# Performance work log

Hardware: AMD Instinct MI355X
Metric: run time of the kernel (lower is better)

## Reference

```python
import jax, jax.numpy as jnp
import numpy as np

H = 1024        # hidden_size
I = 512         # moe_intermediate_size
E = 16          # n_routed_experts
K = 2           # num_experts_per_tok
N_SHARED = 2    # n_shared_experts
IS = I * N_SHARED  # shared expert intermediate
B, S = 2, 2048


def setup_inputs() -> dict:
    key = jax.random.key(0)
    ks = jax.random.split(key, 9)
    sc = 0.02
    return {
        "hidden_states": jax.random.normal(ks[0], (B, S, H), jnp.float32),
        "router_w":     jax.random.normal(ks[1], (E, H), jnp.float32) * sc,
        "expert_gate":  jax.random.normal(ks[2], (E, H, I), jnp.float32) * sc,
        "expert_up":    jax.random.normal(ks[3], (E, H, I), jnp.float32) * sc,
        "expert_down":  jax.random.normal(ks[4], (E, I, H), jnp.float32) * sc,
        "shared_gate":  jax.random.normal(ks[5], (H, IS), jnp.float32) * sc,
        "shared_up":    jax.random.normal(ks[6], (H, IS), jnp.float32) * sc,
        "shared_down":  jax.random.normal(ks[7], (IS, H), jnp.float32) * sc,
    }


def reference(hidden_states, router_w, expert_gate, expert_up, expert_down,
              shared_gate, shared_up, shared_down):
    orig_shape = hidden_states.shape
    x = hidden_states.reshape(-1, H)            # [T, H]
    T = x.shape[0]

    # --- MoEGate: softmax router scores, top-k, normalized weights ---
    scores = jax.nn.softmax(x @ router_w.T, axis=-1)        # [T, E]
    topk_w, topk_idx = jax.lax.top_k(scores, K)             # [T, K]
    topk_w = topk_w / jnp.sum(topk_w, axis=-1, keepdims=True)  # norm_topk_prob

    # Sparse combine weights as dense [T, E] gate matrix (scatter of top-k).
    gates = jnp.zeros((T, E), x.dtype).at[jnp.arange(T)[:, None], topk_idx].add(topk_w)

    # --- Routed experts: gated SiLU MLP per expert, weighted combine ---
    g = jnp.einsum('th,ehi->tei', x, expert_gate)           # [T, E, I]
    u = jnp.einsum('th,ehi->tei', x, expert_up)             # [T, E, I]
    a = jax.nn.silu(g) * u                                  # [T, E, I]
    y = jnp.einsum('tei,eih,te->th', a, expert_down, gates) # [T, H]

    # --- Shared experts ---
    s = (jax.nn.silu(x @ shared_gate) * (x @ shared_up)) @ shared_down  # [T, H]

    return (y + s).reshape(orig_shape)
```

## Files before the change

kernel.cpp:

```cpp
#include <hip/hip_runtime.h>
#include <math.h>

#define H_DIM 1024
#define I_DIM 512
#define E_NUM 16
#define T_TOK 4096
#define IS_DIM 1024
#define CSTR 32

#define P_RT   1024
#define P_WU   (P_RT + 2048)
#define P_SG   (P_WU + 2048)
#define P_SU   (P_SG + 256)
#define P_END  (P_SU + 256)

#define G_TR   2304
#define G_GEMM 1152
#define G_END  (G_TR + G_GEMM)

#define D_GRID 896

typedef unsigned short u16;
typedef __attribute__((ext_vector_type(8))) short short8;
typedef __attribute__((ext_vector_type(4))) float floatx4;

__device__ __forceinline__ float bf2f(u16 u) {
    union { unsigned int u; float f; } c; c.u = ((unsigned int)u) << 16; return c.f;
}
__device__ __forceinline__ u16 f2bf(float f) {
    union { float f; unsigned int u; } c; c.f = f;
    unsigned int r = (c.u + 0x7fffu + ((c.u >> 16) & 1u)) >> 16;
    return (u16)r;
}
__device__ __forceinline__ void gld16(const u16* g, u16* l) {
    __builtin_amdgcn_global_load_lds(
        (const __attribute__((address_space(1))) unsigned int*)g,
        (__attribute__((address_space(3))) unsigned int*)l, 16, 0, 0);
}

__device__ __forceinline__ void tr64(const float* src, u16* dst, int R, int C,
                                     int local, u16* tile)
{
    int tpm = (R >> 6) * (C >> 6);
    int mat = local / tpm;
    int tl_ = local - mat * tpm;
    int tcn = C >> 6;
    int tr = tl_ / tcn, tc = tl_ - tr * tcn;
    src += (size_t)mat * R * C;
    dst += (size_t)mat * R * C;
    int t = threadIdx.x;
    int r0 = t >> 2, c0 = (t & 3) << 4;
    const float* sp = src + (size_t)(tr * 64 + r0) * C + tc * 64 + c0;
    #pragma unroll
    for (int j = 0; j < 16; j += 4) {
        float4 v = *(const float4*)(sp + j);
        tile[r0 * 65 + c0 + j + 0] = f2bf(v.x);
        tile[r0 * 65 + c0 + j + 1] = f2bf(v.y);
        tile[r0 * 65 + c0 + j + 2] = f2bf(v.z);
        tile[r0 * 65 + c0 + j + 3] = f2bf(v.w);
    }
    __syncthreads();
    int cW = t >> 2, rW = (t & 3) << 4;
    u16 tmp[16];
    #pragma unroll
    for (int j = 0; j < 16; ++j) tmp[j] = tile[(rW + j) * 65 + cW];
    u16* dp = dst + (size_t)(tc * 64 + cW) * R + tr * 64 + rW;
    *(uint4*)(dp)     = *(const uint4*)(tmp);
    *(uint4*)(dp + 8) = *(const uint4*)(tmp + 8);
}

__device__ __forceinline__ int derive_routed(int gi, const int* cnt,
                                             int& e, int& mt, int& sub, int& abase)
{
    int off = 0, b = 0;
    #pragma unroll
    for (int ee = 0; ee < E_NUM; ++ee) {
        int mts = (cnt[ee * CSTR] + 127) >> 7;
        int span = mts << 3;
        if (gi < off + span) {
            int local = gi - off;
            e = ee; mt = local >> 3; sub = local & 7; abase = b;
            return 1;
        }
        off += span; b += mts << 7;
    }
    return 0;
}

__global__ __launch_bounds__(256, 4)
void k_prep(const float* x, const float* rw,
            const float* wg, const float* wu, const float* sg, const float* su,
            u16* wgt, u16* wut, u16* sgt, u16* sut,
            u16* xb, float* topkw, int* elist, int* cnt)
{
    __shared__ u16 tile[64 * 65];
    int bi = blockIdx.x;
    if (bi >= P_RT) {
        if (bi < P_WU)      tr64(wg, wgt, 1024, 512,  bi - P_RT, tile);
        else if (bi < P_SG) tr64(wu, wut, 1024, 512,  bi - P_WU, tile);
        else if (bi < P_SU) tr64(sg, sgt, 1024, 1024, bi - P_SG, tile);
        else                tr64(su, sut, 1024, 1024, bi - P_SU, tile);
        return;
    }
    int lane = threadIdx.x & 63;
    int wv = threadIdx.x >> 6;
    int t = bi * 4 + wv;
    const float* xr = x + (size_t)t * H_DIM;
    float xv[16];
    #pragma unroll
    for (int j = 0; j < 16; ++j) xv[j] = xr[j * 64 + lane];
    u16* xrow = xb + (size_t)t * H_DIM;
    #pragma unroll
    for (int j = 0; j < 16; ++j) xrow[j * 64 + lane] = f2bf(xv[j]);
    float sc[E_NUM];
    #pragma unroll
    for (int e = 0; e < E_NUM; ++e) sc[e] = 0.f;
    #pragma unroll
    for (int e = 0; e < E_NUM; ++e) {
        const float* rr = rw + e * H_DIM;
        #pragma unroll
        for (int j = 0; j < 16; ++j) sc[e] += xv[j] * rr[j * 64 + lane];
    }
    #pragma unroll
    for (int off = 32; off > 0; off >>= 1) {
        float tmp[E_NUM];
        #pragma unroll
        for (int e = 0; e < E_NUM; ++e) tmp[e] = __shfl_xor(sc[e], off, 64);
        #pragma unroll
        for (int e = 0; e < E_NUM; ++e) sc[e] += tmp[e];
    }
    if (lane == 0) {
        float b1 = -1e30f, b2 = -1e30f; int i1 = 0, i2 = 0;
        #pragma unroll
        for (int e = 0; e < E_NUM; ++e) {
            if (sc[e] > b1) { b2 = b1; i2 = i1; b1 = sc[e]; i1 = e; }
            else if (sc[e] > b2) { b2 = sc[e]; i2 = e; }
        }
        float w1 = 1.f / (1.f + __expf(b2 - b1));
        float w2 = 1.f - w1;
        topkw[t * 2]     = w1;
        topkw[t * 2 + 1] = w2;
        int p1 = atomicAdd(&cnt[i1 * CSTR], 1); elist[i1 * T_TOK + p1] = (t << 1);
        int p2 = atomicAdd(&cnt[i2 * CSTR], 1); elist[i2 * T_TOK + p2] = (t << 1) | 1;
    }
}

__global__ __launch_bounds__(256, 3)
void k_gateup(const u16* xb, const u16* wgt, const u16* wut,
              const u16* sgt, const u16* sut,
              const float* wd, const float* sd, u16* wdt, u16* sdt,
              const int* elist, const int* cnt,
              u16* act, u16* sact)
{
    __shared__ u16 smem[128 * 64 + 64 * 64 + 64 * 64];
    int bi = blockIdx.x;
    if (bi < G_TR) {
        if (bi < 2048) tr64(wd, wdt, 512, 1024, bi, smem);
        else           tr64(sd, sdt, 1024, 1024, bi - 2048, smem);
        return;
    }
    int gi = bi - G_TR;
    int kind, e = 0, mt, cb, abase = 0;
    if (gi < 512) { kind = 1; mt = gi >> 4; cb = gi & 15; }
    else {
        kind = 0;
        if (!derive_routed(gi - 512, cnt, e, mt, cb, abase)) return;
    }

    u16* lA = smem;
    u16* lG = smem + 8192;
    u16* lU = smem + 12288;
    int tid = threadIdx.x, lane = tid & 63, w = tid >> 6;
    int srow = lane >> 2, scp = lane & 3;

    const u16* gb = kind ? sgt : (wgt + (size_t)e * I_DIM * H_DIM);
    const u16* ub = kind ? sut : (wut + (size_t)e * I_DIM * H_DIM);
    int c = cnt[e * CSTR];

    const u16 *gA[2], *gG, *gU;
    u16 *dA[2], *dG, *dU;
    #pragma unroll
    for (int jj = 0; jj < 2; ++jj) {
        int call = w * 2 + jj;
        int row = call * 16 + srow;
        int gc = scp ^ ((row >> 1) & 3);
        int tok;
        if (kind) tok = mt * 128 + row;
        else {
            int p = mt * 128 + row;
            int pc = p < c ? p : c - 1;
            tok = elist[e * T_TOK + pc] >> 1;
        }
        gA[jj] = xb + (size_t)tok * H_DIM + gc * 8;
        dA[jj] = lA + call * 512;
    }
    {
        int row = w * 16 + srow;
        int gc = scp ^ ((row >> 1) & 3);
        gG = gb + (size_t)(cb * 64 + row) * H_DIM + gc * 8;
        gU = ub + (size_t)(cb * 64 + row) * H_DIM + gc * 8;
        dG = lG + w * 512;
        dU = lU + w * 512;
    }

    int wr = w >> 1, wc = w & 1;
    int quad = lane >> 4, l15 = lane & 15;
    const u16 *fA[4], *fG[2], *fU[2];
    #pragma unroll
    for (int i = 0; i < 4; ++i) {
        int r = wr * 64 + i * 16 + l15;
        fA[i] = lA + r * 32 + (quad ^ ((r >> 1) & 3)) * 8;
    }
    #pragma unroll
    for (int j = 0; j < 2; ++j) {
        int n = wc * 32 + j * 16 + l15;
        fG[j] = lG + n * 32 + (quad ^ ((n >> 1) & 3)) * 8;
        fU[j] = lU + n * 32 + (quad ^ ((n >> 1) & 3)) * 8;
    }

    floatx4 accg[4][2], accu[4][2];
    #pragma unroll
    for (int i = 0; i < 4; ++i)
        #pragma unroll
        for (int j = 0; j < 2; ++j)
            #pragma unroll
            for (int r = 0; r < 4; ++r) { accg[i][j][r] = 0.f; accu[i][j][r] = 0.f; }

    for (int s = 0; s < H_DIM / 64; ++s) {
        #pragma unroll
        for (int q = 0; q < 2; ++q) {
            gld16(gA[0] + q * 32, dA[0] + q * 4096);
            gld16(gA[1] + q * 32, dA[1] + q * 4096);
            gld16(gG + q * 32, dG + q * 2048);
            gld16(gU + q * 32, dU + q * 2048);
        }
        gA[0] += 64; gA[1] += 64; gG += 64; gU += 64;
        __syncthreads();
        #pragma unroll
        for (int q = 0; q < 2; ++q) {
            short8 a[4], g[2], u[2];
            #pragma unroll
            for (int i = 0; i < 4; ++i) a[i] = *(const short8*)(fA[i] + q * 4096);
            #pragma unroll
            for (int j = 0; j < 2; ++j) {
                g[j] = *(const short8*)(fG[j] + q * 2048);
                u[j] = *(const short8*)(fU[j] + q * 2048);
            }
            #pragma unroll
            for (int i = 0; i < 4; ++i)
                #pragma unroll
                for (int j = 0; j < 2; ++j) {
                    accg[i][j] = __builtin_amdgcn_mfma_f32_16x16x32_bf16(a[i], g[j], accg[i][j], 0, 0, 0);
                    accu[i][j] = __builtin_amdgcn_mfma_f32_16x16x32_bf16(a[i], u[j], accu[i][j], 0, 0, 0);
                }
        }
        __syncthreads();
    }

    u16* obase = kind ? (sact + (size_t)(mt * 128) * IS_DIM)
                      : (act + (size_t)(abase + mt * 128) * I_DIM);
    int old = kind ? IS_DIM : I_DIM;
    #pragma unroll
    for (int i = 0; i < 4; ++i)
        #pragma unroll
        for (int j = 0; j < 2; ++j)
            #pragma unroll
            for (int r = 0; r < 4; ++r) {
                int row = wr * 64 + i * 16 + quad * 4 + r;
                int col = cb * 64 + wc * 32 + j * 16 + l15;
                float gg = accg[i][j][r], uu = accu[i][j][r];
                float aa = gg / (1.f + __expf(-gg)) * uu;
                obase[(size_t)row * old + col] = f2bf(aa);
            }
}

__global__ __launch_bounds__(256, 3)
void k_down(const u16* act, const u16* sact, const u16* wdt, const u16* sdt,
            const int* elist, const int* cnt, const float* topkw,
            u16* y0, u16* y1, float* out)
{
    int bi = blockIdx.x;
    int kind, e = 0, mt, nb, abase = 0;
    if (bi < 256) { kind = 1; mt = bi >> 3; nb = bi & 7; }
    else {
        kind = 0;
        if (!derive_routed(bi - 256, cnt, e, mt, nb, abase)) return;
    }

    __shared__ u16 smem[128 * 64 * 2];
    u16* lA = smem;
    u16* lB = smem + 8192;
    int tid = threadIdx.x, lane = tid & 63, w = tid >> 6;
    int srow = lane >> 2, scp = lane & 3;

    int K = kind ? IS_DIM : I_DIM;
    const u16* ab = kind ? (sact + (size_t)(mt * 128) * IS_DIM)
                         : (act + (size_t)(abase + mt * 128) * I_DIM);
    const u16* bb = kind ? (sdt + (size_t)(nb * 128) * IS_DIM)
                         : (wdt + ((size_t)e * H_DIM + nb * 128) * I_DIM);
    int c = cnt[e * CSTR];

    const u16 *gA[2], *gB[2];
    u16 *dA[2], *dB[2];
    #pragma unroll
    for (int jj = 0; jj < 2; ++jj) {
        int call = w * 2 + jj;
        int row = call * 16 + srow;
        int gc = scp ^ ((row >> 1) & 3);
        gA[jj] = ab + (size_t)row * K + gc * 8;
        dA[jj] = lA + call * 512;
        gB[jj] = bb + (size_t)row * K + gc * 8;
        dB[jj] = lB + call * 512;
    }

    int wr = w >> 1, wc = w & 1;
    int quad = lane >> 4, l15 = lane & 15;
    const u16 *fA[4], *fB[4];
    #pragma unroll
    for (int i = 0; i < 4; ++i) {
        int r = wr * 64 + i * 16 + l15;
        fA[i] = lA + r * 32 + (quad ^ ((r >> 1) & 3)) * 8;
    }
    #pragma unroll
    for (int j = 0; j < 4; ++j) {
        int n = wc * 64 + j * 16 + l15;
        fB[j] = lB + n * 32 + (quad ^ ((n >> 1) & 3)) * 8;
    }

    floatx4 acc[4][4];
    #pragma unroll
    for (int i = 0; i < 4; ++i)
        #pragma unroll
        for (int j = 0; j < 4; ++j)
            #pragma unroll
            for (int r = 0; r < 4; ++r) acc[i][j][r] = 0.f;

    int steps = K >> 6;
    for (int s = 0; s < steps; ++s) {
        #pragma unroll
        for (int q = 0; q < 2; ++q) {
            gld16(gA[0] + q * 32, dA[0] + q * 4096);
            gld16(gA[1] + q * 32, dA[1] + q * 4096);
            gld16(gB[0] + q * 32, dB[0] + q * 4096);
            gld16(gB[1] + q * 32, dB[1] + q * 4096);
        }
        gA[0] += 64; gA[1] += 64; gB[0] += 64; gB[1] += 64;
        __syncthreads();
        #pragma unroll
        for (int q = 0; q < 2; ++q) {
            short8 a[4], b[4];
            #pragma unroll
            for (int i = 0; i < 4; ++i) a[i] = *(const short8*)(fA[i] + q * 4096);
            #pragma unroll
            for (int j = 0; j < 4; ++j) b[j] = *(const short8*)(fB[j] + q * 4096);
            #pragma unroll
            for (int i = 0; i < 4; ++i)
                #pragma unroll
                for (int j = 0; j < 4; ++j)
                    acc[i][j] = __builtin_amdgcn_mfma_f32_16x16x32_bf16(a[i], b[j], acc[i][j], 0, 0, 0);
        }
        __syncthreads();
    }

    if (kind) {
        #pragma unroll
        for (int i = 0; i < 4; ++i)
            #pragma unroll
            for (int j = 0; j < 4; ++j)
                #pragma unroll
                for (int r = 0; r < 4; ++r) {
                    int row = mt * 128 + wr * 64 + i * 16 + quad * 4 + r;
                    int col = nb * 128 + wc * 64 + j * 16 + l15;
                    out[(size_t)row * H_DIM + col] = acc[i][j][r];
                }
    } else {
        #pragma unroll
        for (int i = 0; i < 4; ++i)
            #pragma unroll
            for (int r = 0; r < 4; ++r) {
                int row = wr * 64 + i * 16 + quad * 4 + r;
                int p = mt * 128 + row;
                if (p < c) {
                    int ent = elist[e * T_TOK + p];
                    int t = ent >> 1, sl = ent & 1;
                    float wt = topkw[t * 2 + sl];
                    u16* yb = sl ? y1 : y0;
                    #pragma unroll
                    for (int j = 0; j < 4; ++j) {
                        int col = nb * 128 + wc * 64 + j * 16 + l15;
                        yb[(size_t)t * H_DIM + col] = f2bf(wt * acc[i][j][r]);
                    }
                }
            }
    }
}

__global__ __launch_bounds__(256)
void k_final(float* out, const u16* y0, const u16* y1)
{
    int i = blockIdx.x * 256 + threadIdx.x;
    float4 o = ((const float4*)out)[i];
    uint2 a = ((const uint2*)y0)[i];
    uint2 b = ((const uint2*)y1)[i];
    const u16* pa = (const u16*)&a;
    const u16* pb = (const u16*)&b;
    o.x += bf2f(pa[0]) + bf2f(pb[0]);
    o.y += bf2f(pa[1]) + bf2f(pb[1]);
    o.z += bf2f(pa[2]) + bf2f(pb[2]);
    o.w += bf2f(pa[3]) + bf2f(pb[3]);
    ((float4*)out)[i] = o;
}

extern "C" void kernel_launch(void* const* d_in, const int* in_sizes, int n_in,
                              void* d_out, int out_size, void* d_ws, size_t ws_size,
                              hipStream_t stream)
{
    const float* x  = (const float*)d_in[0];
    const float* rw = (const float*)d_in[1];
    const float* wg = (const float*)d_in[2];
    const float* wu = (const float*)d_in[3];
    const float* wd = (const float*)d_in[4];
    const float* sg = (const float*)d_in[5];
    const float* su = (const float*)d_in[6];
    const float* sd = (const float*)d_in[7];
    float* out = (float*)d_out;

    char* ws = (char*)d_ws;
    const size_t MB = 1024ull * 1024ull;
    u16* wgt  = (u16*)(ws);
    u16* wut  = (u16*)(ws + 16 * MB);
    u16* wdt  = (u16*)(ws + 32 * MB);
    u16* sgt  = (u16*)(ws + 48 * MB);
    u16* sut  = (u16*)(ws + 50 * MB);
    u16* sdt  = (u16*)(ws + 52 * MB);
    u16* xb   = (u16*)(ws + 54 * MB);
    u16* act  = (u16*)(ws + 62 * MB);
    u16* sact = (u16*)(ws + 72 * MB);
    u16* y0   = (u16*)(ws + 80 * MB);
    u16* y1   = (u16*)(ws + 88 * MB);
    float* topkw  = (float*)(ws + 96 * MB);
    int* elist    = (int*)(ws + 96 * MB + 64 * 1024);
    int* cnt      = (int*)(ws + 97 * MB);

    hipMemsetAsync(cnt, 0, E_NUM * CSTR * sizeof(int), stream);
    k_prep<<<P_END, 256, 0, stream>>>(x, rw, wg, wu, sg, su,
                                      wgt, wut, sgt, sut,
                                      xb, topkw, elist, cnt);
    k_gateup<<<G_END, 256, 0, stream>>>(xb, wgt, wut, sgt, sut,
                                        wd, sd, wdt, sdt,
                                        elist, cnt, act, sact);
    k_down<<<D_GRID, 256, 0, stream>>>(act, sact, wdt, sdt,
                                       elist, cnt, topkw, y0, y1, out);
    k_final<<<T_TOK * H_DIM / 4 / 256, 256, 0, stream>>>(out, y0, y1);
}
```

Baseline: 273.5 us.

## Double-buffer LDS tiles in gate/up and down GEMMs, reorder transpose blocks

Both GEMM kernels now stage the next K-slice into a second LDS buffer while MFMAs consume the current one, so global-to-LDS loads can overlap compute and one barrier per step is removed. LDS grows to 64KB per block and launch bounds drop from 3 to 2 blocks per CU. The gate/up kernel also moves the weight-transpose blocks to the end of the grid, so GEMM blocks get scheduled first. The cost is lower occupancy.

Measured after the change: 278.2 us. About the same (+1.7%).

```diff
diff --git a/kernel.cpp b/kernel.cpp
--- a/kernel.cpp
+++ b/kernel.cpp
@@ -14,9 +14,9 @@
 #define P_SU   (P_SG + 256)
 #define P_END  (P_SU + 256)
 
+#define G_GEMM 1152
 #define G_TR   2304
-#define G_GEMM 1152
-#define G_END  (G_TR + G_GEMM)
+#define G_END  (G_GEMM + G_TR)
 
 #define D_GRID 896
 
@@ -145,31 +145,28 @@
     }
 }
 
-__global__ __launch_bounds__(256, 3)
+__global__ __launch_bounds__(256, 2)
 void k_gateup(const u16* xb, const u16* wgt, const u16* wut,
               const u16* sgt, const u16* sut,
               const float* wd, const float* sd, u16* wdt, u16* sdt,
               const int* elist, const int* cnt,
               u16* act, u16* sact)
 {
-    __shared__ u16 smem[128 * 64 + 64 * 64 + 64 * 64];
+    __shared__ u16 smem[32768];
     int bi = blockIdx.x;
-    if (bi < G_TR) {
-        if (bi < 2048) tr64(wd, wdt, 512, 1024, bi, smem);
-        else           tr64(sd, sdt, 1024, 1024, bi - 2048, smem);
+    if (bi >= G_GEMM) {
+        int tb = bi - G_GEMM;
+        if (tb < 2048) tr64(wd, wdt, 512, 1024, tb, smem);
+        else           tr64(sd, sdt, 1024, 1024, tb - 2048, smem);
         return;
     }
-    int gi = bi - G_TR;
     int kind, e = 0, mt, cb, abase = 0;
-    if (gi < 512) { kind = 1; mt = gi >> 4; cb = gi & 15; }
+    if (bi < 512) { kind = 1; mt = bi >> 4; cb = bi & 15; }
     else {
         kind = 0;
-        if (!derive_routed(gi - 512, cnt, e, mt, cb, abase)) return;
-    }
-
-    u16* lA = smem;
-    u16* lG = smem + 8192;
-    u16* lU = smem + 12288;
+        if (!derive_routed(bi - 512, cnt, e, mt, cb, abase)) return;
+    }
+
     int tid = threadIdx.x, lane = tid & 63, w = tid >> 6;
     int srow = lane >> 2, scp = lane & 3;
 
@@ -177,45 +174,46 @@
     const u16* ub = kind ? sut : (wut + (size_t)e * I_DIM * H_DIM);
     int c = cnt[e * CSTR];
 
-    const u16 *gA[2], *gG, *gU;
-    u16 *dA[2], *dG, *dU;
-    #pragma unroll
-    for (int jj = 0; jj < 2; ++jj) {
-        int call = w * 2 + jj;
-        int row = call * 16 + srow;
-        int gc = scp ^ ((row >> 1) & 3);
-        int tok;
-        if (kind) tok = mt * 128 + row;
+    const u16 *gA0, *gA1, *gG, *gU;
+    int oA0, oA1, oG, oU;
+    {
+        int row0 = (w * 2) * 16 + srow;
+        int row1 = (w * 2 + 1) * 16 + srow;
+        int gc0 = scp ^ ((row0 >> 1) & 3);
+        int gc1 = scp ^ ((row1 >> 1) & 3);
+        int tok0, tok1;
+        if (kind) { tok0 = mt * 128 + row0; tok1 = mt * 128 + row1; }
         else {
-            int p = mt * 128 + row;
-            int pc = p < c ? p : c - 1;
-            tok = elist[e * T_TOK + pc] >> 1;
+            int p0 = mt * 128 + row0; int pc0 = p0 < c ? p0 : c - 1;
+            int p1 = mt * 128 + row1; int pc1 = p1 < c ? p1 : c - 1;
+            tok0 = elist[e * T_TOK + pc0] >> 1;
+            tok1 = elist[e * T_TOK + pc1] >> 1;
         }
-        gA[jj] = xb + (size_t)tok * H_DIM + gc * 8;
-        dA[jj] = lA + call * 512;
-    }
-    {
-        int row = w * 16 + srow;
-        int gc = scp ^ ((row >> 1) & 3);
-        gG = gb + (size_t)(cb * 64 + row) * H_DIM + gc * 8;
-        gU = ub + (size_t)(cb * 64 + row) * H_DIM + gc * 8;
-        dG = lG + w * 512;
-        dU = lU + w * 512;
+        gA0 = xb + (size_t)tok0 * H_DIM + gc0 * 8;
+        gA1 = xb + (size_t)tok1 * H_DIM + gc1 * 8;
+        oA0 = (w * 2) * 512;
+        oA1 = (w * 2 + 1) * 512;
+        int rw_ = w * 16 + srow;
+        int gcw = scp ^ ((rw_ >> 1) & 3);
+        gG = gb + (size_t)(cb * 64 + rw_) * H_DIM + gcw * 8;
+        gU = ub + (size_t)(cb * 64 + rw_) * H_DIM + gcw * 8;
+        oG = 8192 + w * 512;
+        oU = 12288 + w * 512;
     }
 
     int wr = w >> 1, wc = w & 1;
     int quad = lane >> 4, l15 = lane & 15;
-    const u16 *fA[4], *fG[2], *fU[2];
+    int fA[4], fG[2], fU[2];
     #pragma unroll
     for (int i = 0; i < 4; ++i) {
         int r = wr * 64 + i * 16 + l15;
-        fA[i] = lA + r * 32 + (quad ^ ((r >> 1) & 3)) * 8;
+        fA[i] = r * 32 + (quad ^ ((r >> 1) & 3)) * 8;
     }
     #pragma unroll
     for (int j = 0; j < 2; ++j) {
         int n = wc * 32 + j * 16 + l15;
-        fG[j] = lG + n * 32 + (quad ^ ((n >> 1) & 3)) * 8;
-        fU[j] = lU + n * 32 + (quad ^ ((n >> 1) & 3)) * 8;
+        fG[j] = 8192  + n * 32 + (quad ^ ((n >> 1) & 3)) * 8;
+        fU[j] = 12288 + n * 32 + (quad ^ ((n >> 1) & 3)) * 8;
     }
 
     floatx4 accg[4][2], accu[4][2];
@@ -226,25 +224,32 @@
             #pragma unroll
             for (int r = 0; r < 4; ++r) { accg[i][j][r] = 0.f; accu[i][j][r] = 0.f; }
 
+#define STAGE_GU(bsel) { \
+    u16* sb = smem + (bsel) * 16384; \
+    _Pragma("unroll") \
+    for (int q = 0; q < 2; ++q) { \
+        gld16(gA0 + q * 32, sb + oA0 + q * 4096); \
+        gld16(gA1 + q * 32, sb + oA1 + q * 4096); \
+        gld16(gG  + q * 32, sb + oG  + q * 2048); \
+        gld16(gU  + q * 32, sb + oU  + q * 2048); \
+    } \
+    gA0 += 64; gA1 += 64; gG += 64; gU += 64; }
+
+    STAGE_GU(0);
+    __syncthreads();
     for (int s = 0; s < H_DIM / 64; ++s) {
-        #pragma unroll
-        for (int q = 0; q < 2; ++q) {
-            gld16(gA[0] + q * 32, dA[0] + q * 4096);
-            gld16(gA[1] + q * 32, dA[1] + q * 4096);
-            gld16(gG + q * 32, dG + q * 2048);
-            gld16(gU + q * 32, dU + q * 2048);
-        }
-        gA[0] += 64; gA[1] += 64; gG += 64; gU += 64;
-        __syncthreads();
+        int cur = s & 1;
+        if (s + 1 < H_DIM / 64) STAGE_GU(cur ^ 1);
+        const u16* cbuf = smem + cur * 16384;
         #pragma unroll
         for (int q = 0; q < 2; ++q) {
             short8 a[4], g[2], u[2];
             #pragma unroll
-            for (int i = 0; i < 4; ++i) a[i] = *(const short8*)(fA[i] + q * 4096);
+            for (int i = 0; i < 4; ++i) a[i] = *(const short8*)(cbuf + fA[i] + q * 4096);
             #pragma unroll
             for (int j = 0; j < 2; ++j) {
-                g[j] = *(const short8*)(fG[j] + q * 2048);
-                u[j] = *(const short8*)(fU[j] + q * 2048);
+                g[j] = *(const short8*)(cbuf + fG[j] + q * 2048);
+                u[j] = *(const short8*)(cbuf + fU[j] + q * 2048);
             }
             #pragma unroll
             for (int i = 0; i < 4; ++i)
@@ -256,6 +261,7 @@
         }
         __syncthreads();
     }
+#undef STAGE_GU
 
     u16* obase = kind ? (sact + (size_t)(mt * 128) * IS_DIM)
                       : (act + (size_t)(abase + mt * 128) * I_DIM);
@@ -274,7 +280,7 @@
             }
 }
 
-__global__ __launch_bounds__(256, 3)
+__global__ __launch_bounds__(256, 2)
 void k_down(const u16* act, const u16* sact, const u16* wdt, const u16* sdt,
             const int* elist, const int* cnt, const float* topkw,
             u16* y0, u16* y1, float* out)
@@ -287,9 +293,7 @@
         if (!derive_routed(bi - 256, cnt, e, mt, nb, abase)) return;
     }
 
-    __shared__ u16 smem[128 * 64 * 2];
-    u16* lA = smem;
-    u16* lB = smem + 8192;
+    __shared__ u16 smem[32768];
     int tid = threadIdx.x, lane = tid & 63, w = tid >> 6;
     int srow = lane >> 2, scp = lane & 3;
 
@@ -300,31 +304,35 @@
                          : (wdt + ((size_t)e * H_DIM + nb * 128) * I_DIM);
     int c = cnt[e * CSTR];
 
-    const u16 *gA[2], *gB[2];
-    u16 *dA[2], *dB[2];
-    #pragma unroll
-    for (int jj = 0; jj < 2; ++jj) {
-        int call = w * 2 + jj;
-        int row = call * 16 + srow;
-        int gc = scp ^ ((row >> 1) & 3);
-        gA[jj] = ab + (size_t)row * K + gc * 8;
-        dA[jj] = lA + call * 512;
-        gB[jj] = bb + (size_t)row * K + gc * 8;
-        dB[jj] = lB + call * 512;
+    const u16 *gA0, *gA1, *gB0, *gB1;
+    int oA0, oA1, oB0, oB1;
+    {
+        int row0 = (w * 2) * 16 + srow;
+        int row1 = (w * 2 + 1) * 16 + srow;
+        int gc0 = scp ^ ((row0 >> 1) & 3);
+        int gc1 = scp ^ ((row1 >> 1) & 3);
+        gA0 = ab + (size_t)row0 * K + gc0 * 8;
+        gA1 = ab + (size_t)row1 * K + gc1 * 8;
+        gB0 = bb + (size_t)row0 * K + gc0 * 8;
+        gB1 = bb + (size_t)row1 * K + gc1 * 8;
+        oA0 = (w * 2) * 512;
+        oA1 = (w * 2 + 1) * 512;
+        oB0 = 8192 + (w * 2) * 512;
+        oB1 = 8192 + (w * 2 + 1) * 512;
     }
 
     int wr = w >> 1, wc = w & 1;
     int quad = lane >> 4, l15 = lane & 15;
-    const u16 *fA[4], *fB[4];
+    int fA[4], fB[4];
     #pragma unroll
     for (int i = 0; i < 4; ++i) {
         int r = wr * 64 + i * 16 + l15;
-        fA[i] = lA + r * 32 + (quad ^ ((r >> 1) & 3)) * 8;
+        fA[i] = r * 32 + (quad ^ ((r >> 1) & 3)) * 8;
     }
     #pragma unroll
     for (int j = 0; j < 4; ++j) {
         int n = wc * 64 + j * 16 + l15;
-        fB[j] = lB + n * 32 + (quad ^ ((n >> 1) & 3)) * 8;
+        fB[j] = 8192 + n * 32 + (quad ^ ((n >> 1) & 3)) * 8;
     }
 
     floatx4 acc[4][4];
@@ -335,24 +343,31 @@
             #pragma unroll
             for (int r = 0; r < 4; ++r) acc[i][j][r] = 0.f;
 
+#define STAGE_DN(bsel) { \
+    u16* sb = smem + (bsel) * 16384; \
+    _Pragma("unroll") \
+    for (int q = 0; q < 2; ++q) { \
+        gld16(gA0 + q * 32, sb + oA0 + q * 4096); \
+        gld16(gA1 + q * 32, sb + oA1 + q * 4096); \
+        gld16(gB0 + q * 32, sb + oB0 + q * 4096); \
+        gld16(gB1 + q * 32, sb + oB1 + q * 4096); \
+    } \
+    gA0 += 64; gA1 += 64; gB0 += 64; gB1 += 64; }
+
     int steps = K >> 6;
+    STAGE_DN(0);
+    __syncthreads();
     for (int s = 0; s < steps; ++s) {
-        #pragma unroll
-        for (int q = 0; q < 2; ++q) {
-            gld16(gA[0] + q * 32, dA[0] + q * 4096);
-            gld16(gA[1] + q * 32, dA[1] + q * 4096);
-            gld16(gB[0] + q * 32, dB[0] + q * 4096);
-            gld16(gB[1] + q * 32, dB[1] + q * 4096);
-        }
-        gA[0] += 64; gA[1] += 64; gB[0] += 64; gB[1] += 64;
-        __syncthreads();
+        int cur = s & 1;
+        if (s + 1 < steps) STAGE_DN(cur ^ 1);
+        const u16* cbuf = smem + cur * 16384;
         #pragma unroll
         for (int q = 0; q < 2; ++q) {
             short8 a[4], b[4];
             #pragma unroll
-            for (int i = 0; i < 4; ++i) a[i] = *(const short8*)(fA[i] + q * 4096);
-            #pragma unroll
-            for (int j = 0; j < 4; ++j) b[j] = *(const short8*)(fB[j] + q * 4096);
+            for (int i = 0; i < 4; ++i) a[i] = *(const short8*)(cbuf + fA[i] + q * 4096);
+            #pragma unroll
+            for (int j = 0; j < 4; ++j) b[j] = *(const short8*)(cbuf + fB[j] + q * 4096);
             #pragma unroll
             for (int i = 0; i < 4; ++i)
                 #pragma unroll
@@ -361,6 +376,7 @@
         }
         __syncthreads();
     }
+#undef STAGE_DN
 
     if (kind) {
         #pragma unroll
```

## Use 256x256 tiles with double-buffered staged MFMA pipeline in gate-up and down GEMMs

Applied to the files above, without the earlier changes.

Rewrites the gate/up and down GEMM kernels to use 512-thread blocks with 256-row by 128/256-column tiles. Global-to-LDS loads are double-buffered and split into four quarter stages, with explicit vmcnt waits, barriers, sched barriers and setprio around the MFMA bursts. The weight-transpose blocks switch to 128x128 tiles, and routed tiles are padded to 256 rows with guarded stores. This targets better operand reuse and overlap of loads with compute, at the cost of fewer blocks, more padding waste for small experts, and fragile hand-tuned wait counts.

Result: slower. 279.4 us (+2.2%).

```diff
diff --git a/kernel.cpp b/kernel.cpp
--- a/kernel.cpp
+++ b/kernel.cpp
@@ -14,15 +14,23 @@
 #define P_SU   (P_SG + 256)
 #define P_END  (P_SU + 256)
 
-#define G_TR   2304
-#define G_GEMM 1152
-#define G_END  (G_TR + G_GEMM)
-
-#define D_GRID 896
+#define G_GEMM 352
+#define G_TR   576
+#define G_END  (G_GEMM + G_TR)
+
+#define D_GRID 288
 
 typedef unsigned short u16;
 typedef __attribute__((ext_vector_type(8))) short short8;
 typedef __attribute__((ext_vector_type(4))) float floatx4;
+
+#define VM0   asm volatile("s_waitcnt vmcnt(0)" ::: "memory")
+#define VM2   asm volatile("s_waitcnt vmcnt(2)" ::: "memory")
+#define VM4   asm volatile("s_waitcnt vmcnt(4)" ::: "memory")
+#define VM6   asm volatile("s_waitcnt vmcnt(6)" ::: "memory")
+#define LGKM0 asm volatile("s_waitcnt lgkmcnt(0)" ::: "memory")
+#define BAR   __builtin_amdgcn_s_barrier()
+#define SCHB  __builtin_amdgcn_sched_barrier(0)
 
 __device__ __forceinline__ float bf2f(u16 u) {
     union { unsigned int u; float f; } c; c.u = ((unsigned int)u) << 16; return c.f;
@@ -69,20 +77,55 @@
     *(uint4*)(dp + 8) = *(const uint4*)(tmp + 8);
 }
 
-__device__ __forceinline__ int derive_routed(int gi, const int* cnt,
-                                             int& e, int& mt, int& sub, int& abase)
+__device__ __forceinline__ void tr128(const float* src, u16* dst, int R, int C,
+                                      int local, u16* tile )
+{
+    int tpm = (R >> 7) * (C >> 7);
+    int mat = local / tpm;
+    int tl_ = local - mat * tpm;
+    int tcn = C >> 7;
+    int tr = tl_ / tcn, tc = tl_ - tr * tcn;
+    src += (size_t)mat * R * C;
+    dst += (size_t)mat * R * C;
+    int t = threadIdx.x;
+    int r0 = t >> 2, c0 = (t & 3) << 5;
+    const float* sp = src + (size_t)(tr * 128 + r0) * C + tc * 128 + c0;
+    #pragma unroll
+    for (int j = 0; j < 32; j += 4) {
+        float4 v = *(const float4*)(sp + j);
+        tile[r0 * 129 + c0 + j + 0] = f2bf(v.x);
+        tile[r0 * 129 + c0 + j + 1] = f2bf(v.y);
+        tile[r0 * 129 + c0 + j + 2] = f2bf(v.z);
+        tile[r0 * 129 + c0 + j + 3] = f2bf(v.w);
+    }
+    __syncthreads();
+    int cW = t >> 2, rW = (t & 3) << 5;
+    u16 tmp[32];
+    #pragma unroll
+    for (int j = 0; j < 32; ++j) tmp[j] = tile[(rW + j) * 129 + cW];
+    u16* dp = dst + (size_t)(tc * 128 + cW) * R + tr * 128 + rW;
+    *(uint4*)(dp)      = *(const uint4*)(tmp);
+    *(uint4*)(dp + 8)  = *(const uint4*)(tmp + 8);
+    *(uint4*)(dp + 16) = *(const uint4*)(tmp + 16);
+    *(uint4*)(dp + 24) = *(const uint4*)(tmp + 24);
+}
+
+__device__ __forceinline__ int derive256(int gi, const int* cnt,
+        int& e, int& mt, int& sub, int& abase, int& rowsE)
 {
     int off = 0, b = 0;
     #pragma unroll
     for (int ee = 0; ee < E_NUM; ++ee) {
-        int mts = (cnt[ee * CSTR] + 127) >> 7;
-        int span = mts << 3;
+        int cc = cnt[ee * CSTR];
+        int rE = ((cc + 127) >> 7) << 7;
+        int mts = (rE + 255) >> 8;
+        int span = mts << 2;
         if (gi < off + span) {
             int local = gi - off;
-            e = ee; mt = local >> 3; sub = local & 7; abase = b;
+            e = ee; mt = local >> 2; sub = local & 3; abase = b; rowsE = rE;
             return 1;
         }
-        off += span; b += mts << 7;
+        off += span; b += rE;
     }
     return 0;
 }
@@ -145,250 +188,302 @@
     }
 }
 
-__global__ __launch_bounds__(256, 3)
+#define STG(part, buf, tt) { \
+    u16* d_ = sm + (buf) * 32768 + (part) * 8192 + w * 512; \
+    gld16(pst[part][0] + (tt) * 64, d_); \
+    gld16(pst[part][1] + (tt) * 64, d_ + 4096); }
+
+#define RD(o) (*(const short8*)(sm + bsel * 32768 + (o)))
+
+#define MM16(ACC, AA, J0) \
+    _Pragma("unroll") \
+    for (int mi = 0; mi < 4; ++mi) \
+        _Pragma("unroll") \
+        for (int j = 0; j < 2; ++j) \
+            _Pragma("unroll") \
+            for (int kh = 0; kh < 2; ++kh) \
+                ACC[mi][j] = __builtin_amdgcn_mfma_f32_16x16x32_bf16( \
+                    AA[mi][kh], bq[(J0) + j][kh], ACC[mi][j], 0, 0, 0);
+
+__global__ __launch_bounds__(512, 2)
 void k_gateup(const u16* xb, const u16* wgt, const u16* wut,
               const u16* sgt, const u16* sut,
               const float* wd, const float* sd, u16* wdt, u16* sdt,
               const int* elist, const int* cnt,
               u16* act, u16* sact)
 {
-    __shared__ u16 smem[128 * 64 + 64 * 64 + 64 * 64];
+    __shared__ u16 sm[65536];
     int bi = blockIdx.x;
-    if (bi < G_TR) {
-        if (bi < 2048) tr64(wd, wdt, 512, 1024, bi, smem);
-        else           tr64(sd, sdt, 1024, 1024, bi - 2048, smem);
+    if (bi >= G_GEMM) {
+        int tb = bi - G_GEMM;
+        if (tb < 512) tr128(wd, wdt, 512, 1024, tb, sm);
+        else          tr128(sd, sdt, 1024, 1024, tb - 512, sm);
         return;
     }
-    int gi = bi - G_TR;
-    int kind, e = 0, mt, cb, abase = 0;
-    if (gi < 512) { kind = 1; mt = gi >> 4; cb = gi & 15; }
-    else {
-        kind = 0;
-        if (!derive_routed(gi - 512, cnt, e, mt, cb, abase)) return;
-    }
-
-    u16* lA = smem;
-    u16* lG = smem + 8192;
-    u16* lU = smem + 12288;
+    int kind, e = 0, mt, cb, abase = 0, rowsE = 0;
+    if (bi < 128) { kind = 1; mt = bi >> 3; cb = bi & 7; }
+    else { kind = 0; if (!derive256(bi - 128, cnt, e, mt, cb, abase, rowsE)) return; }
+
     int tid = threadIdx.x, lane = tid & 63, w = tid >> 6;
-    int srow = lane >> 2, scp = lane & 3;
+    int wr = w >> 2, wc = w & 3;
+    int quad = lane >> 4, l15 = lane & 15;
+    int l8r = lane >> 3, l8c = lane & 7;
+    int sg = (l8c ^ l8r) * 8;
+    int c = kind ? 0 : cnt[e * CSTR];
 
     const u16* gb = kind ? sgt : (wgt + (size_t)e * I_DIM * H_DIM);
     const u16* ub = kind ? sut : (wut + (size_t)e * I_DIM * H_DIM);
-    int c = cnt[e * CSTR];
-
-    const u16 *gA[2], *gG, *gU;
-    u16 *dA[2], *dG, *dU;
-    #pragma unroll
-    for (int jj = 0; jj < 2; ++jj) {
-        int call = w * 2 + jj;
-        int row = call * 16 + srow;
-        int gc = scp ^ ((row >> 1) & 3);
-        int tok;
-        if (kind) tok = mt * 128 + row;
-        else {
-            int p = mt * 128 + row;
-            int pc = p < c ? p : c - 1;
-            tok = elist[e * T_TOK + pc] >> 1;
-        }
-        gA[jj] = xb + (size_t)tok * H_DIM + gc * 8;
-        dA[jj] = lA + call * 512;
-    }
-    {
-        int row = w * 16 + srow;
-        int gc = scp ^ ((row >> 1) & 3);
-        gG = gb + (size_t)(cb * 64 + row) * H_DIM + gc * 8;
-        gU = ub + (size_t)(cb * 64 + row) * H_DIM + gc * 8;
-        dG = lG + w * 512;
-        dU = lU + w * 512;
-    }
-
-    int wr = w >> 1, wc = w & 1;
-    int quad = lane >> 4, l15 = lane & 15;
-    const u16 *fA[4], *fG[2], *fU[2];
-    #pragma unroll
-    for (int i = 0; i < 4; ++i) {
-        int r = wr * 64 + i * 16 + l15;
-        fA[i] = lA + r * 32 + (quad ^ ((r >> 1) & 3)) * 8;
-    }
-    #pragma unroll
-    for (int j = 0; j < 2; ++j) {
-        int n = wc * 32 + j * 16 + l15;
-        fG[j] = lG + n * 32 + (quad ^ ((n >> 1) & 3)) * 8;
-        fU[j] = lU + n * 32 + (quad ^ ((n >> 1) & 3)) * 8;
-    }
-
-    floatx4 accg[4][2], accu[4][2];
-    #pragma unroll
-    for (int i = 0; i < 4; ++i)
+
+    const u16* pst[4][2];
+    #pragma unroll
+    for (int part = 0; part < 2; ++part)
+        #pragma unroll
+        for (int l = 0; l < 2; ++l) {
+            int R = part * 128 + l * 64 + w * 8 + l8r;
+            int tok;
+            if (kind) tok = mt * 256 + R;
+            else { int p = mt * 256 + R; int pc = p < c ? p : c - 1;
+                   tok = elist[e * T_TOK + pc] >> 1; }
+            pst[part][l] = xb + (size_t)tok * H_DIM + sg;
+        }
+    #pragma unroll
+    for (int l = 0; l < 2; ++l) {
+        int n = cb * 128 + l * 64 + w * 8 + l8r;
+        pst[2][l] = gb + (size_t)n * H_DIM + sg;
+        pst[3][l] = ub + (size_t)n * H_DIM + sg;
+    }
+
+    int slot0 = (quad ^ (l15 & 7)) * 8;
+    int slot1 = ((4 + quad) ^ (l15 & 7)) * 8;
+    int baseA0 = wr * 8192 + l15 * 64 + slot0;
+    int baseA1 = wr * 8192 + l15 * 64 + slot1;
+    int baseB0 = 16384 + wc * 2048 + l15 * 64 + slot0;
+    int baseB1 = 16384 + wc * 2048 + l15 * 64 + slot1;
+
+    floatx4 accL[8][2], accU[8][2];
+    #pragma unroll
+    for (int i = 0; i < 8; ++i)
         #pragma unroll
         for (int j = 0; j < 2; ++j)
             #pragma unroll
-            for (int r = 0; r < 4; ++r) { accg[i][j][r] = 0.f; accu[i][j][r] = 0.f; }
-
-    for (int s = 0; s < H_DIM / 64; ++s) {
-        #pragma unroll
-        for (int q = 0; q < 2; ++q) {
-            gld16(gA[0] + q * 32, dA[0] + q * 4096);
-            gld16(gA[1] + q * 32, dA[1] + q * 4096);
-            gld16(gG + q * 32, dG + q * 2048);
-            gld16(gU + q * 32, dU + q * 2048);
-        }
-        gA[0] += 64; gA[1] += 64; gG += 64; gU += 64;
-        __syncthreads();
-        #pragma unroll
-        for (int q = 0; q < 2; ++q) {
-            short8 a[4], g[2], u[2];
-            #pragma unroll
-            for (int i = 0; i < 4; ++i) a[i] = *(const short8*)(fA[i] + q * 4096);
-            #pragma unroll
-            for (int j = 0; j < 2; ++j) {
-                g[j] = *(const short8*)(fG[j] + q * 2048);
-                u[j] = *(const short8*)(fU[j] + q * 2048);
-            }
-            #pragma unroll
-            for (int i = 0; i < 4; ++i)
-                #pragma unroll
-                for (int j = 0; j < 2; ++j) {
-                    accg[i][j] = __builtin_amdgcn_mfma_f32_16x16x32_bf16(a[i], g[j], accg[i][j], 0, 0, 0);
-                    accu[i][j] = __builtin_amdgcn_mfma_f32_16x16x32_bf16(a[i], u[j], accu[i][j], 0, 0, 0);
-                }
-        }
-        __syncthreads();
-    }
-
-    u16* obase = kind ? (sact + (size_t)(mt * 128) * IS_DIM)
-                      : (act + (size_t)(abase + mt * 128) * I_DIM);
-    int old = kind ? IS_DIM : I_DIM;
-    #pragma unroll
-    for (int i = 0; i < 4; ++i)
+            for (int r = 0; r < 4; ++r) { accL[i][j][r] = 0.f; accU[i][j][r] = 0.f; }
+    short8 a0[4][2], a1[4][2], bq[4][2];
+
+    STG(0, 0, 0); STG(1, 0, 0); STG(2, 0, 0); STG(3, 0, 0); STG(0, 1, 1);
+    VM4; BAR;
+
+    const int nt = H_DIM / 64;
+    for (int t = 0; t < nt; ++t) {
+        int bsel = t & 1, bnx = bsel ^ 1;
+        bool last = (t == nt - 1), pen = (t == nt - 2);
+        if (!last) STG(1, bnx, t + 1);
+        #pragma unroll
+        for (int mi = 0; mi < 4; ++mi) {
+            a0[mi][0] = RD(baseA0 + mi * 1024);
+            a0[mi][1] = RD(baseA1 + mi * 1024);
+        }
+        #pragma unroll
+        for (int j = 0; j < 2; ++j) {
+            bq[j][0] = RD(baseB0 + j * 1024);
+            bq[j][1] = RD(baseB1 + j * 1024);
+        }
+        if (last) { VM0; } else { VM4; }
+        BAR; LGKM0; SCHB;
+        __builtin_amdgcn_s_setprio(1);
+        MM16(accL, a0, 0);
+        __builtin_amdgcn_s_setprio(0);
+        SCHB; BAR;
+        if (!last) STG(2, bnx, t + 1);
+        #pragma unroll
+        for (int j = 0; j < 2; ++j) {
+            bq[2 + j][0] = RD(baseB0 + 8192 + j * 1024);
+            bq[2 + j][1] = RD(baseB1 + 8192 + j * 1024);
+        }
+        if (last) { VM0; } else { VM6; }
+        BAR; LGKM0; SCHB;
+        __builtin_amdgcn_s_setprio(1);
+        MM16(accU, a0, 2);
+        __builtin_amdgcn_s_setprio(0);
+        SCHB; BAR;
+        if (!last) STG(3, bnx, t + 1);
+        #pragma unroll
+        for (int mi = 0; mi < 4; ++mi) {
+            a1[mi][0] = RD(baseA0 + 4096 + mi * 1024);
+            a1[mi][1] = RD(baseA1 + 4096 + mi * 1024);
+        }
+        if (last) { VM0; } else { VM6; }
+        BAR; LGKM0; SCHB;
+        __builtin_amdgcn_s_setprio(1);
+        MM16((&accL[4]), a1, 0);
+        __builtin_amdgcn_s_setprio(0);
+        SCHB; BAR;
+        if (t + 2 < nt) STG(0, bsel, t + 2);
+        if (last) { VM0; } else if (pen) { VM2; } else { VM4; }
+        BAR; LGKM0; SCHB;
+        __builtin_amdgcn_s_setprio(1);
+        MM16((&accU[4]), a1, 2);
+        __builtin_amdgcn_s_setprio(0);
+        SCHB; BAR;
+    }
+
+    u16* ob; int ostride;
+    if (kind) { ob = sact + (size_t)(mt * 256) * IS_DIM; ostride = IS_DIM; }
+    else      { ob = act + (size_t)(abase + mt * 256) * I_DIM; ostride = I_DIM; }
+    #pragma unroll
+    for (int mi = 0; mi < 8; ++mi)
         #pragma unroll
         for (int j = 0; j < 2; ++j)
             #pragma unroll
             for (int r = 0; r < 4; ++r) {
-                int row = wr * 64 + i * 16 + quad * 4 + r;
-                int col = cb * 64 + wc * 32 + j * 16 + l15;
-                float gg = accg[i][j][r], uu = accu[i][j][r];
+                int row = wr * 128 + mi * 16 + quad * 4 + r;
+                int col = cb * 128 + wc * 32 + j * 16 + l15;
+                float gg = accL[mi][j][r], uu = accU[mi][j][r];
                 float aa = gg / (1.f + __expf(-gg)) * uu;
-                obase[(size_t)row * old + col] = f2bf(aa);
+                if (kind || (mt * 256 + row < rowsE))
+                    ob[(size_t)row * ostride + col] = f2bf(aa);
             }
 }
 
-__global__ __launch_bounds__(256, 3)
+__global__ __launch_bounds__(512, 2)
 void k_down(const u16* act, const u16* sact, const u16* wdt, const u16* sdt,
             const int* elist, const int* cnt, const float* topkw,
             u16* y0, u16* y1, float* out)
 {
+    __shared__ u16 sm[65536];
     int bi = blockIdx.x;
-    int kind, e = 0, mt, nb, abase = 0;
-    if (bi < 256) { kind = 1; mt = bi >> 3; nb = bi & 7; }
-    else {
-        kind = 0;
-        if (!derive_routed(bi - 256, cnt, e, mt, nb, abase)) return;
-    }
-
-    __shared__ u16 smem[128 * 64 * 2];
-    u16* lA = smem;
-    u16* lB = smem + 8192;
+    int kind, e = 0, mt, nb, abase = 0, rowsE = 0;
+    if (bi < 64) { kind = 1; mt = bi >> 2; nb = bi & 3; }
+    else { kind = 0; if (!derive256(bi - 64, cnt, e, mt, nb, abase, rowsE)) return; }
+
     int tid = threadIdx.x, lane = tid & 63, w = tid >> 6;
-    int srow = lane >> 2, scp = lane & 3;
+    int wr = w >> 2, wc = w & 3;
+    int quad = lane >> 4, l15 = lane & 15;
+    int l8r = lane >> 3, l8c = lane & 7;
+    int sg = (l8c ^ l8r) * 8;
+    int c = kind ? 0 : cnt[e * CSTR];
 
     int K = kind ? IS_DIM : I_DIM;
-    const u16* ab = kind ? (sact + (size_t)(mt * 128) * IS_DIM)
-                         : (act + (size_t)(abase + mt * 128) * I_DIM);
-    const u16* bb = kind ? (sdt + (size_t)(nb * 128) * IS_DIM)
-                         : (wdt + ((size_t)e * H_DIM + nb * 128) * I_DIM);
-    int c = cnt[e * CSTR];
-
-    const u16 *gA[2], *gB[2];
-    u16 *dA[2], *dB[2];
-    #pragma unroll
-    for (int jj = 0; jj < 2; ++jj) {
-        int call = w * 2 + jj;
-        int row = call * 16 + srow;
-        int gc = scp ^ ((row >> 1) & 3);
-        gA[jj] = ab + (size_t)row * K + gc * 8;
-        dA[jj] = lA + call * 512;
-        gB[jj] = bb + (size_t)row * K + gc * 8;
-        dB[jj] = lB + call * 512;
-    }
-
-    int wr = w >> 1, wc = w & 1;
-    int quad = lane >> 4, l15 = lane & 15;
-    const u16 *fA[4], *fB[4];
-    #pragma unroll
-    for (int i = 0; i < 4; ++i) {
-        int r = wr * 64 + i * 16 + l15;
-        fA[i] = lA + r * 32 + (quad ^ ((r >> 1) & 3)) * 8;
-    }
-    #pragma unroll
-    for (int j = 0; j < 4; ++j) {
-        int n = wc * 64 + j * 16 + l15;
-        fB[j] = lB + n * 32 + (quad ^ ((n >> 1) & 3)) * 8;
-    }
-
-    floatx4 acc[4][4];
-    #pragma unroll
-    for (int i = 0; i < 4; ++i)
-        #pragma unroll
-        for (int j = 0; j < 4; ++j)
+    const u16* ab = kind ? (sact + (size_t)(mt * 256) * IS_DIM)
+                         : (act + (size_t)(abase + mt * 256) * I_DIM);
+    const u16* bb = kind ? sdt : (wdt + (size_t)e * H_DIM * I_DIM);
+
+    const u16* pst[4][2];
+    #pragma unroll
+    for (int part = 0; part < 2; ++part)
+        #pragma unroll
+        for (int l = 0; l < 2; ++l) {
+            int R = part * 128 + l * 64 + w * 8 + l8r;
+            pst[part][l] = ab + (size_t)R * K + sg;
+        }
+    #pragma unroll
+    for (int l = 0; l < 2; ++l) {
+        int n = nb * 256 + l * 64 + w * 8 + l8r;
+        pst[2][l] = bb + (size_t)n * K + sg;
+        pst[3][l] = bb + (size_t)(n + 128) * K + sg;
+    }
+
+    int slot0 = (quad ^ (l15 & 7)) * 8;
+    int slot1 = ((4 + quad) ^ (l15 & 7)) * 8;
+    int baseA0 = wr * 8192 + l15 * 64 + slot0;
+    int baseA1 = wr * 8192 + l15 * 64 + slot1;
+    int baseB0 = 16384 + wc * 2048 + l15 * 64 + slot0;
+    int baseB1 = 16384 + wc * 2048 + l15 * 64 + slot1;
+
+    floatx4 accL[8][2], accU[8][2];
+    #pragma unroll
+    for (int i = 0; i < 8; ++i)
+        #pragma unroll
+        for (int j = 0; j < 2; ++j)
             #pragma unroll
-            for (int r = 0; r < 4; ++r) acc[i][j][r] = 0.f;
-
-    int steps = K >> 6;
-    for (int s = 0; s < steps; ++s) {
-        #pragma unroll
-        for (int q = 0; q < 2; ++q) {
-            gld16(gA[0] + q * 32, dA[0] + q * 4096);
-            gld16(gA[1] + q * 32, dA[1] + q * 4096);
-            gld16(gB[0] + q * 32, dB[0] + q * 4096);
-            gld16(gB[1] + q * 32, dB[1] + q * 4096);
-        }
-        gA[0] += 64; gA[1] += 64; gB[0] += 64; gB[1] += 64;
-        __syncthreads();
-        #pragma unroll
-        for (int q = 0; q < 2; ++q) {
-            short8 a[4], b[4];
-            #pragma unroll
-            for (int i = 0; i < 4; ++i) a[i] = *(const short8*)(fA[i] + q * 4096);
-            #pragma unroll
-            for (int j = 0; j < 4; ++j) b[j] = *(const short8*)(fB[j] + q * 4096);
-            #pragma unroll
-            for (int i = 0; i < 4; ++i)
-                #pragma unroll
-                for (int j = 0; j < 4; ++j)
-                    acc[i][j] = __builtin_amdgcn_mfma_f32_16x16x32_bf16(a[i], b[j], acc[i][j], 0, 0, 0);
-        }
-        __syncthreads();
+            for (int r = 0; r < 4; ++r) { accL[i][j][r] = 0.f; accU[i][j][r] = 0.f; }
+    short8 a0[4][2], a1[4][2], bq[4][2];
+
+    STG(0, 0, 0); STG(1, 0, 0); STG(2, 0, 0); STG(3, 0, 0); STG(0, 1, 1);
+    VM4; BAR;
+
+    const int nt = K >> 6;
+    for (int t = 0; t < nt; ++t) {
+        int bsel = t & 1, bnx = bsel ^ 1;
+        bool last = (t == nt - 1), pen = (t == nt - 2);
+        if (!last) STG(1, bnx, t + 1);
+        #pragma unroll
+        for (int mi = 0; mi < 4; ++mi) {
+            a0[mi][0] = RD(baseA0 + mi * 1024);
+            a0[mi][1] = RD(baseA1 + mi * 1024);
+        }
+        #pragma unroll
+        for (int j = 0; j < 2; ++j) {
+            bq[j][0] = RD(baseB0 + j * 1024);
+            bq[j][1] = RD(baseB1 + j * 1024);
+        }
+        if (last) { VM0; } else { VM4; }
+        BAR; LGKM0; SCHB;
+        __builtin_amdgcn_s_setprio(1);
+        MM16(accL, a0, 0);
+        __builtin_amdgcn_s_setprio(0);
+        SCHB; BAR;
+        if (!last) STG(2, bnx, t + 1);
+        #pragma unroll
+        for (int j = 0; j < 2; ++j) {
+            bq[2 + j][0] = RD(baseB0 + 8192 + j * 1024);
+            bq[2 + j][1] = RD(baseB1 + 8192 + j * 1024);
+        }
+        if (last) { VM0; } else { VM6; }
+        BAR; LGKM0; SCHB;
+        __builtin_amdgcn_s_setprio(1);
+        MM16(accU, a0, 2);
+        __builtin_amdgcn_s_setprio(0);
+        SCHB; BAR;
+        if (!last) STG(3, bnx, t + 1);
+        #pragma unroll
+        for (int mi = 0; mi < 4; ++mi) {
+            a1[mi][0] = RD(baseA0 + 4096 + mi * 1024);
+            a1[mi][1] = RD(baseA1 + 4096 + mi * 1024);
+        }
+        if (last) { VM0; } else { VM6; }
+        BAR; LGKM0; SCHB;
+        __builtin_amdgcn_s_setprio(1);
+        MM16((&accL[4]), a1, 0);
+        __builtin_amdgcn_s_setprio(0);
+        SCHB; BAR;
+        if (t + 2 < nt) STG(0, bsel, t + 2);
+        if (last) { VM0; } else if (pen) { VM2; } else { VM4; }
+        BAR; LGKM0; SCHB;
+        __builtin_amdgcn_s_setprio(1);
+        MM16((&accU[4]), a1, 2);
+        __builtin_amdgcn_s_setprio(0);
+        SCHB; BAR;
     }
 
     if (kind) {
         #pragma unroll
-        for (int i = 0; i < 4; ++i)
-            #pragma unroll
-            for (int j = 0; j < 4; ++j)
-                #pragma unroll
-                for (int r = 0; r < 4; ++r) {
-                    int row = mt * 128 + wr * 64 + i * 16 + quad * 4 + r;
-                    int col = nb * 128 + wc * 64 + j * 16 + l15;
-                    out[(size_t)row * H_DIM + col] = acc[i][j][r];
-                }
-    } else {
-        #pragma unroll
-        for (int i = 0; i < 4; ++i)
+        for (int mi = 0; mi < 8; ++mi)
             #pragma unroll
             for (int r = 0; r < 4; ++r) {
-                int row = wr * 64 + i * 16 + quad * 4 + r;
-                int p = mt * 128 + row;
+                int row = mt * 256 + wr * 128 + mi * 16 + quad * 4 + r;
+                #pragma unroll
+                for (int j = 0; j < 2; ++j) {
+                    out[(size_t)row * H_DIM + nb * 256 + wc * 32 + j * 16 + l15] = accL[mi][j][r];
+                    out[(size_t)row * H_DIM + nb * 256 + 128 + wc * 32 + j * 16 + l15] = accU[mi][j][r];
+                }
+            }
+    } else {
+        #pragma unroll
+        for (int mi = 0; mi < 8; ++mi)
+            #pragma unroll
+            for (int r = 0; r < 4; ++r) {
+                int p = mt * 256 + wr * 128 + mi * 16 + quad * 4 + r;
                 if (p < c) {
                     int ent = elist[e * T_TOK + p];
-                    int t = ent >> 1, sl = ent & 1;
-                    float wt = topkw[t * 2 + sl];
+                    int tok = ent >> 1, sl = ent & 1;
+                    float wt = topkw[tok * 2 + sl];
                     u16* yb = sl ? y1 : y0;
                     #pragma unroll
-                    for (int j = 0; j < 4; ++j) {
-                        int col = nb * 128 + wc * 64 + j * 16 + l15;
-                        yb[(size_t)t * H_DIM + col] = f2bf(wt * acc[i][j][r]);
+                    for (int j = 0; j < 2; ++j) {
+                        yb[(size_t)tok * H_DIM + nb * 256 + wc * 32 + j * 16 + l15] =
+                            f2bf(wt * accL[mi][j][r]);
+                        yb[(size_t)tok * H_DIM + nb * 256 + 128 + wc * 32 + j * 16 + l15] =
+                            f2bf(wt * accU[mi][j][r]);
                     }
                 }
             }
@@ -435,21 +530,21 @@
     u16* sdt  = (u16*)(ws + 52 * MB);
     u16* xb   = (u16*)(ws + 54 * MB);
     u16* act  = (u16*)(ws + 62 * MB);
-    u16* sact = (u16*)(ws + 72 * MB);
-    u16* y0   = (u16*)(ws + 80 * MB);
-    u16* y1   = (u16*)(ws + 88 * MB);
-    float* topkw  = (float*)(ws + 96 * MB);
-    int* elist    = (int*)(ws + 96 * MB + 64 * 1024);
-    int* cnt      = (int*)(ws + 97 * MB);
+    u16* sact = (u16*)(ws + 74 * MB);
+    u16* y0   = (u16*)(ws + 82 * MB);
+    u16* y1   = (u16*)(ws + 90 * MB);
+    float* topkw  = (float*)(ws + 98 * MB);
+    int* elist    = (int*)(ws + 98 * MB + 64 * 1024);
+    int* cnt      = (int*)(ws + 98 * MB + 512 * 1024);
 
     hipMemsetAsync(cnt, 0, E_NUM * CSTR * sizeof(int), stream);
     k_prep<<<P_END, 256, 0, stream>>>(x, rw, wg, wu, sg, su,
                                       wgt, wut, sgt, sut,
                                       xb, topkw, elist, cnt);
-    k_gateup<<<G_END, 256, 0, stream>>>(xb, wgt, wut, sgt, sut,
+    k_gateup<<<G_END, 512, 0, stream>>>(xb, wgt, wut, sgt, sut,
                                         wd, sd, wdt, sdt,
                                         elist, cnt, act, sact);
-    k_down<<<D_GRID, 256, 0, stream>>>(act, sact, wdt, sdt,
+    k_down<<<D_GRID, 512, 0, stream>>>(act, sact, wdt, sdt,
                                        elist, cnt, topkw, y0, y1, out);
     k_final<<<T_TOK * H_DIM / 4 / 256, 256, 0, stream>>>(out, y0, y1);
 }
```
